# Performance work log

Hardware: AMD Instinct MI355X
Metric: run time of the kernel (lower is better)

## Reference

```python
import jax, jax.numpy as jnp
import numpy as np

NUM_LEVELS = 1000
DIMENSIONS = 10000


def setup_inputs() -> dict:
    key = jax.random.key(0)
    k1, k2, k3, k4 = jax.random.split(key, 4)
    x = jax.random.uniform(k1, (32, 1, 28, 28), dtype=jnp.float32)  # MNIST-like, values in [0,1)
    # torchhd Random / Level hypervectors are +/-1 (MAP VSA)
    pos_weight = jnp.where(jax.random.normal(k2, (784, DIMENSIONS)) > 0, 1.0, -1.0).astype(jnp.float32)
    level_weight = jnp.where(jax.random.normal(k3, (NUM_LEVELS, DIMENSIONS)) > 0, 1.0, -1.0).astype(jnp.float32)
    classify_weight = jax.random.normal(k4, (10, DIMENSIONS), dtype=jnp.float32) * 0.01
    return {"x": x, "pos_weight": pos_weight, "level_weight": level_weight,
            "classify_weight": classify_weight}


def reference(x, pos_weight, level_weight, classify_weight):
    B = x.shape[0]
    xf = x.reshape(B, -1)  # flatten -> [B, 784]
    # Level embedding: quantize value in [0,1] to nearest of NUM_LEVELS indices
    idx = jnp.clip(jnp.round(xf * (NUM_LEVELS - 1)), 0, NUM_LEVELS - 1).astype(jnp.int32)
    levels = jnp.take(level_weight, idx, axis=0)  # [B, 784, D] gather
    # bind (elementwise mult with position HVs) + multiset (sum over pixels)
    hv = jnp.einsum('pd,bpd->bd', pos_weight, levels)  # [B, D]
    # hard_quantize: sign with 0 -> -1
    enc = jnp.where(hv > 0, 1.0, -1.0).astype(hv.dtype)
    logit = enc @ classify_weight.T  # [B, num_classes]
    return logit
```

## Files before the change

kernel.cpp:

```cpp
#include <hip/hip_runtime.h>
#include <stdint.h>

#define D    10000
#define P    784
#define B    32
#define NL   1000
#define NC   10

#define ROWW 320
#define ROWB (ROWW * 4)
#define NW   313
#define CHUNKS 8
#define PLEN  98
#define PLANES 7

#define OFFS_OFF  0
#define LVL_OFF   (B * P * 4)
#define POS_OFF   (LVL_OFF + NL * ROWB)
#define PART_OFF  (POS_OFF + P * ROWB)

__global__ void k_idx(const float* __restrict__ x, int* __restrict__ offs,
                      float* __restrict__ out) {
    int i = blockIdx.x * 256 + threadIdx.x;
    if (i < B * P) {
        float v = rintf(x[i] * 999.0f);
        v = fminf(fmaxf(v, 0.0f), 999.0f);
        offs[i] = (int)v * ROWB;
    }
    if (i < B * NC) out[i] = 0.0f;
}

__global__ void k_pack(const float* __restrict__ lvl, const float* __restrict__ pos,
                       uint32_t* __restrict__ lvl_b, uint32_t* __restrict__ pos_b) {
    int bx  = blockIdx.x;
    int row = bx / 40;
    int seg = bx % 40;
    int d   = seg * 256 + threadIdx.x;
    const float* src; uint32_t* dst;
    if (row < NL) { src = lvl + (size_t)row * D;        dst = lvl_b + (size_t)row * ROWW; }
    else          { src = pos + (size_t)(row - NL) * D; dst = pos_b + (size_t)(row - NL) * ROWW; }
    float v = (d < D) ? src[d] : 1.0f;
    unsigned long long m = __ballot(v < 0.0f);
    if ((threadIdx.x & 63) == 0) {
        *(uint2*)(dst + (d >> 5)) = make_uint2((uint32_t)m, (uint32_t)(m >> 32));
    }
}

__global__ __launch_bounds__(64) void k_bind(const int* __restrict__ offs,
                                             const uint32_t* __restrict__ lvl_b,
                                             const uint32_t* __restrict__ pos_b,
                                             uint32_t* __restrict__ part) {
    int b = blockIdx.z, c = blockIdx.y;
    int w = blockIdx.x * 64 + threadIdx.x;
    const int* po = offs + b * P + c * PLEN;
    const uint32_t* pb = pos_b + (size_t)(c * PLEN) * ROWW + w;
    const char* lb = (const char*)lvl_b;
    int wb = w << 2;

    uint32_t pl[PLANES];
    #pragma unroll
    for (int k = 0; k < PLANES; k++) pl[k] = 0;

    #pragma unroll 7
    for (int i = 0; i < PLEN; i += 2) {
        int o0 = po[i], o1 = po[i + 1];
        uint32_t l0 = *(const uint32_t*)(lb + o0 + wb);
        uint32_t l1 = *(const uint32_t*)(lb + o1 + wb);
        uint32_t x0 = l0 ^ pb[(size_t)i * ROWW];
        uint32_t x1 = l1 ^ pb[(size_t)(i + 1) * ROWW];
        uint32_t t  = x0 ^ x1;
        uint32_t cr = (x0 & x1) | (pl[0] & t);
        pl[0] ^= t;
        #pragma unroll
        for (int k = 1; k < PLANES; k++) { uint32_t tt = pl[k] & cr; pl[k] ^= cr; cr = tt; }
    }
    uint32_t* pp = part + (size_t)((b * CHUNKS + c) * PLANES) * ROWW + w;
    #pragma unroll
    for (int k = 0; k < PLANES; k++) pp[(size_t)k * ROWW] = pl[k];
}

template <int N>
__device__ inline void bsadd(const uint32_t* a, const uint32_t* b, uint32_t* s) {
    uint32_t cin = 0;
    #pragma unroll
    for (int k = 0; k < N; k++) {
        uint32_t t = a[k] ^ b[k];
        s[k] = t ^ cin;
        cin  = (a[k] & b[k]) | (cin & t);
    }
    s[N] = cin;
}

__global__ __launch_bounds__(64) void k_cls(const uint32_t* __restrict__ part,
                                            const float* __restrict__ cw,
                                            float* __restrict__ out) {
    int b = blockIdx.y;
    int w = blockIdx.x * 64 + threadIdx.x;
    float acc[NC];
    #pragma unroll
    for (int c = 0; c < NC; c++) acc[c] = 0.0f;

    if (w < NW) {
        uint32_t ch[CHUNKS][PLANES];
        #pragma unroll
        for (int c = 0; c < CHUNKS; c++)
            #pragma unroll
            for (int k = 0; k < PLANES; k++)
                ch[c][k] = part[(size_t)((b * CHUNKS + c) * PLANES + k) * ROWW + w];

        uint32_t s01[8], s23[8], s45[8], s67[8], t0[9], t1[9], s[10];
        bsadd<7>(ch[0], ch[1], s01);
        bsadd<7>(ch[2], ch[3], s23);
        bsadd<7>(ch[4], ch[5], s45);
        bsadd<7>(ch[6], ch[7], s67);
        bsadd<8>(s01, s23, t0);
        bsadd<8>(s45, s67, t1);
        bsadd<9>(t0, t1, s);
        uint32_t minus = s[9] | (s[8] & s[7] & (s[3] | s[4] | s[5] | s[6]));

        float sgn[32];
        #pragma unroll
        for (int j = 0; j < 32; j++) sgn[j] = ((minus >> j) & 1u) ? -1.0f : 1.0f;

        const float* wp = cw + w * 32;
        if (w < NW - 1) {
            #pragma unroll
            for (int c = 0; c < NC; c++) {
                const float* r = wp + c * D;
                float a = 0.0f;
                #pragma unroll
                for (int j = 0; j < 32; j++) a = fmaf(sgn[j], r[j], a);
                acc[c] = a;
            }
        } else {
            #pragma unroll
            for (int c = 0; c < NC; c++) {
                const float* r = wp + c * D;
                float a = 0.0f;
                #pragma unroll
                for (int j = 0; j < 16; j++) a = fmaf(sgn[j], r[j], a);
                acc[c] = a;
            }
        }
    }
    #pragma unroll
    for (int c = 0; c < NC; c++) {
        float v = acc[c];
        for (int o = 32; o > 0; o >>= 1) v += __shfl_down(v, o, 64);
        if (threadIdx.x == 0) atomicAdd(out + b * NC + c, v);
    }
}

extern "C" void kernel_launch(void* const* d_in, const int* in_sizes, int n_in,
                              void* d_out, int out_size, void* d_ws, size_t ws_size,
                              hipStream_t stream) {
    const float* x   = (const float*)d_in[0];
    const float* pos = (const float*)d_in[1];
    const float* lvl = (const float*)d_in[2];
    const float* cw  = (const float*)d_in[3];
    float* out = (float*)d_out;

    char* ws = (char*)d_ws;
    int*       offs  = (int*)(ws + OFFS_OFF);
    uint32_t*  lvl_b = (uint32_t*)(ws + LVL_OFF);
    uint32_t*  pos_b = (uint32_t*)(ws + POS_OFF);
    uint32_t*  part  = (uint32_t*)(ws + PART_OFF);

    k_idx <<<dim3((B * P + 255) / 256), 256, 0, stream>>>(x, offs, out);
    k_pack<<<dim3((NL + P) * 40),       256, 0, stream>>>(lvl, pos, lvl_b, pos_b);
    k_bind<<<dim3(5, CHUNKS, B),         64, 0, stream>>>(offs, lvl_b, pos_b, part);
    k_cls <<<dim3(5, B),                 64, 0, stream>>>(part, cw, out);
}
```

Baseline: 139.9 us.

## Fuse index kernel into pack, vectorize packing, and drop atomics in classifier

Merges the index-quantization kernel into the packing kernel, which now loads float4 per thread and assembles 32-bit sign words with shuffles, using 4x fewer blocks. The classifier now runs one 320-thread block per batch row and reduces through shared memory, writing outputs directly instead of using atomics, so the output zeroing is no longer needed. The aim is to cut one launch, reduce the number of pack blocks and make its memory accesses wider, and remove atomic contention. In exchange, k_cls has only 32 blocks, which leaves little parallelism.

```diff
diff --git a/kernel.cpp b/kernel.cpp
--- a/kernel.cpp
+++ b/kernel.cpp
@@ -19,30 +19,41 @@
 #define POS_OFF   (LVL_OFF + NL * ROWB)
 #define PART_OFF  (POS_OFF + P * ROWB)
 
-__global__ void k_idx(const float* __restrict__ x, int* __restrict__ offs,
-                      float* __restrict__ out) {
-    int i = blockIdx.x * 256 + threadIdx.x;
-    if (i < B * P) {
+#define PACK_BPR 10
+
+__global__ void k_pack(const float* __restrict__ x,
+                       const float* __restrict__ lvl, const float* __restrict__ pos,
+                       int* __restrict__ offs,
+                       uint32_t* __restrict__ lvl_b, uint32_t* __restrict__ pos_b) {
+    int bx  = blockIdx.x;
+    int row = bx / PACK_BPR;
+    int seg = bx % PACK_BPR;
+    int d0  = seg * 1024 + threadIdx.x * 4;
+    const float* src; uint32_t* dst;
+    if (row < NL) { src = lvl + (size_t)row * D;        dst = lvl_b + (size_t)row * ROWW; }
+    else          { src = pos + (size_t)(row - NL) * D; dst = pos_b + (size_t)(row - NL) * ROWW; }
+
+    uint32_t nib = 0;
+    if (d0 < D) {
+        float4 v = *(const float4*)(src + d0);
+        nib = (v.x < 0.0f ? 1u : 0u) | (v.y < 0.0f ? 2u : 0u) |
+              (v.z < 0.0f ? 4u : 0u) | (v.w < 0.0f ? 8u : 0u);
+    }
+    int lane = threadIdx.x & 63;
+    uint32_t val = nib << ((lane & 7) * 4);
+    val |= __shfl_xor(val, 1, 64);
+    val |= __shfl_xor(val, 2, 64);
+    val |= __shfl_xor(val, 4, 64);
+    if ((lane & 7) == 0) {
+        int gword = (seg * 1024 + (threadIdx.x & ~7) * 4) >> 5;
+        dst[gword] = val;
+    }
+
+    if (bx < 98) {
+        int i = bx * 256 + threadIdx.x;
         float v = rintf(x[i] * 999.0f);
         v = fminf(fmaxf(v, 0.0f), 999.0f);
         offs[i] = (int)v * ROWB;
-    }
-    if (i < B * NC) out[i] = 0.0f;
-}
-
-__global__ void k_pack(const float* __restrict__ lvl, const float* __restrict__ pos,
-                       uint32_t* __restrict__ lvl_b, uint32_t* __restrict__ pos_b) {
-    int bx  = blockIdx.x;
-    int row = bx / 40;
-    int seg = bx % 40;
-    int d   = seg * 256 + threadIdx.x;
-    const float* src; uint32_t* dst;
-    if (row < NL) { src = lvl + (size_t)row * D;        dst = lvl_b + (size_t)row * ROWW; }
-    else          { src = pos + (size_t)(row - NL) * D; dst = pos_b + (size_t)(row - NL) * ROWW; }
-    float v = (d < D) ? src[d] : 1.0f;
-    unsigned long long m = __ballot(v < 0.0f);
-    if ((threadIdx.x & 63) == 0) {
-        *(uint2*)(dst + (d >> 5)) = make_uint2((uint32_t)m, (uint32_t)(m >> 32));
     }
 }
 
@@ -91,11 +102,11 @@
     s[N] = cin;
 }
 
-__global__ __launch_bounds__(64) void k_cls(const uint32_t* __restrict__ part,
-                                            const float* __restrict__ cw,
-                                            float* __restrict__ out) {
-    int b = blockIdx.y;
-    int w = blockIdx.x * 64 + threadIdx.x;
+__global__ __launch_bounds__(320) void k_cls(const uint32_t* __restrict__ part,
+                                             const float* __restrict__ cw,
+                                             float* __restrict__ out) {
+    int b = blockIdx.x;
+    int w = threadIdx.x;
     float acc[NC];
     #pragma unroll
     for (int c = 0; c < NC; c++) acc[c] = 0.0f;
@@ -123,7 +134,8 @@
         for (int j = 0; j < 32; j++) sgn[j] = ((minus >> j) & 1u) ? -1.0f : 1.0f;
 
         const float* wp = cw + w * 32;
-        if (w < NW - 1) {
+        int lim = (w < NW - 1) ? 32 : 16;
+        if (lim == 32) {
             #pragma unroll
             for (int c = 0; c < NC; c++) {
                 const float* r = wp + c * D;
@@ -143,11 +155,20 @@
             }
         }
     }
+
+    __shared__ float red[5][NC];
+    int wave = threadIdx.x >> 6, lane = threadIdx.x & 63;
     #pragma unroll
     for (int c = 0; c < NC; c++) {
         float v = acc[c];
         for (int o = 32; o > 0; o >>= 1) v += __shfl_down(v, o, 64);
-        if (threadIdx.x == 0) atomicAdd(out + b * NC + c, v);
+        if (lane == 0) red[wave][c] = v;
+    }
+    __syncthreads();
+    if (threadIdx.x < NC) {
+        float ssum = red[0][threadIdx.x] + red[1][threadIdx.x] + red[2][threadIdx.x]
+                   + red[3][threadIdx.x] + red[4][threadIdx.x];
+        out[b * NC + threadIdx.x] = ssum;
     }
 }
 
@@ -166,8 +187,7 @@
     uint32_t*  pos_b = (uint32_t*)(ws + POS_OFF);
     uint32_t*  part  = (uint32_t*)(ws + PART_OFF);
 
-    k_idx <<<dim3((B * P + 255) / 256), 256, 0, stream>>>(x, offs, out);
-    k_pack<<<dim3((NL + P) * 40),       256, 0, stream>>>(lvl, pos, lvl_b, pos_b);
+    k_pack<<<dim3((NL + P) * PACK_BPR), 256, 0, stream>>>(x, lvl, pos, offs, lvl_b, pos_b);
     k_bind<<<dim3(5, CHUNKS, B),         64, 0, stream>>>(offs, lvl_b, pos_b, part);
-    k_cls <<<dim3(5, B),                 64, 0, stream>>>(part, cw, out);
+    k_cls <<<dim3(B),                   320, 0, stream>>>(part, cw, out);
 }
```

Result: faster. 127.7 us (-8.8%).
